# Performance work log

Hardware: AMD Instinct MI355X
Metric: run time of the kernel (lower is better)

Reference implementation:

```python
import math
import jax, jax.numpy as jnp
import numpy as np
from jax import lax

RAY_START, RAY_END = 0.5, 2.5
N_PLANES = 32

# ---- camera constants (faithful to pose_spherical / fibonacci_sphere / ImagePlanes init) ----

def _pose_spherical_np(theta, phi, radius):
    trans_t = np.array([[1,0,0,0],[0,1,0,0],[0,0,1,radius],[0,0,0,1]], dtype=np.float64)
    p = phi/180.0*np.pi
    rot_phi = np.array([[1,0,0,0],[0,np.cos(p),-np.sin(p),0],[0,np.sin(p),np.cos(p),0],[0,0,0,1]], dtype=np.float64)
    t = theta/180.0*np.pi
    rot_theta = np.array([[np.cos(t),0,-np.sin(t),0],[0,1,0,0],[np.sin(t),0,np.cos(t),0],[0,0,0,1]], dtype=np.float64)
    e = 90.0/180.0*np.pi
    rot_eta = np.array([[np.cos(e),np.sin(e),0,0],[-np.sin(e),np.cos(e),0,0],[0,0,1,0],[0,0,0,1]], dtype=np.float64)
    c2w = rot_eta @ (rot_theta @ (rot_phi @ trans_t))
    return np.array([[-1,0,0,0],[0,0,1,0],[0,1,0,0],[0,0,0,1]], dtype=np.float64) @ c2w

def _fibonacci_sphere(n):
    pts = []
    golden = math.pi*(math.sqrt(5.0)-1.0)
    for i in range(n):
        y = 1 - (i/float(n-1))*2
        r = math.sqrt(1-y*y)
        th = golden*i
        x, z = math.cos(th)*r, math.sin(th)*r
        pts.append((math.atan2(z, math.sqrt(x*x+y*y)), math.atan2(y, x)))
    return pts

_poses = np.stack([_pose_spherical_np(theta, phi, -1.307) for phi, theta in _fibonacci_sphere(N_PLANES)])
_flip = np.diag(np.array([-1.0,1.0,1.0,1.0]))
POSES34 = jnp.asarray(np.stack([np.linalg.inv(p @ _flip)[:3] for p in _poses]).astype(np.float32))  # [32,3,4]
KMAT = jnp.asarray(np.array([[1.0254,0,0.5],[0,1.0254,0.5],[0,0,1]], dtype=np.float32))  # [3,3]

# ---- grid_sample(bilinear, zeros, align_corners=False) ----

def _grid_sample(img, grid):
    # img [C,H,W], grid [P,2] (x,y) in [-1,1] -> [C,P]
    C, H, W = img.shape
    ix = ((grid[:, 0] + 1.0)*W - 1.0)*0.5
    iy = ((grid[:, 1] + 1.0)*H - 1.0)*0.5
    x0 = jnp.floor(ix); y0 = jnp.floor(iy)
    wx1 = ix - x0; wy1 = iy - y0
    def tap(xx, yy, w):
        valid = (xx >= 0) & (xx <= W - 1) & (yy >= 0) & (yy <= H - 1)
        xi = jnp.clip(xx, 0, W - 1).astype(jnp.int32)
        yi = jnp.clip(yy, 0, H - 1).astype(jnp.int32)
        return img[:, yi, xi] * (w*valid)[None, :]
    return (tap(x0, y0, (1-wx1)*(1-wy1)) + tap(x0+1, y0, wx1*(1-wy1))
            + tap(x0, y0+1, (1-wx1)*wy1) + tap(x0+1, y0+1, wx1*wy1))

# ---- ImagePlanes.forward ----

def _image_plane_feats(images, points):
    # images [32,3,H,W], points [P,3] -> [P, 96+64]
    P = points.shape[0]
    ph = jnp.concatenate([points, jnp.ones((P, 1), points.dtype)], axis=1)  # [P,4]
    cam = jnp.einsum('kij,pj->kip', POSES34, ph)            # [32,3,P]
    ps = jnp.einsum('ij,kjp->kip', KMAT, cam)                # [32,3,P]
    pix = jnp.clip(ps[:, :2, :] / ps[:, 2:3, :], 0.0, 1.0)*2.0 - 1.0  # [32,2,P]
    grid = jnp.transpose(pix, (0, 2, 1))                     # [32,P,2]
    feats = jax.vmap(_grid_sample)(images, grid)             # [32,3,P]
    feats = jnp.transpose(feats, (2, 0, 1)).reshape(P, -1)   # [P,96] plane-major
    pixflat = jnp.transpose(grid, (1, 0, 2)).reshape(P, -1)  # [P,64]
    return jnp.concatenate([feats, pixflat], axis=1)

# ---- RenderNetwork.forward (only self.net path is used) ----

def _decode(x, W1, b1, W2, b2):
    h = jax.nn.softplus(x @ W1 + b1)
    o = h @ W2 + b2
    rgb = jax.nn.sigmoid(o[..., 1:])*(1.0 + 2*0.001) - 0.001
    return rgb, o[..., 0:1]

# ---- MipRayMarcher2 ----

def _ray_march(colors, densities, depths):
    deltas = depths[:, :, 1:] - depths[:, :, :-1]
    cm = (colors[:, :, :-1] + colors[:, :, 1:])*0.5
    dm = (densities[:, :, :-1] + densities[:, :, 1:])*0.5
    zm = (depths[:, :, :-1] + depths[:, :, 1:])*0.5
    dm = jax.nn.softplus(dm - 1.0)
    alpha = 1.0 - jnp.exp(-dm*deltas)
    shifted = jnp.concatenate([jnp.ones_like(alpha[:, :, :1]), 1.0 - alpha + 1e-10], axis=2)
    weights = alpha * jnp.cumprod(shifted, axis=2)[:, :, :-1]
    rgb = jnp.sum(weights*cm, axis=2)*2.0 - 1.0
    wtot = jnp.sum(weights, axis=2)
    depth = jnp.sum(weights*zm, axis=2)/wtot
    depth = jnp.clip(jnp.where(jnp.isnan(depth), jnp.inf, depth), jnp.min(depths), jnp.max(depths))
    return rgb, depth, weights

# ---- importance sampling (sample_pdf + maxpool/avgpool smoothing) ----

def _sample_pdf(bins, weights, u, eps=1e-5):
    M = weights.shape[-1]
    weights = weights + eps
    pdf = weights / jnp.sum(weights, -1, keepdims=True)
    cdf = jnp.cumsum(pdf, -1)
    cdf = jnp.concatenate([jnp.zeros_like(cdf[:, :1]), cdf], -1)  # [R,M+1]
    inds = jax.vmap(lambda c, uu: jnp.searchsorted(c, uu, side='right'))(cdf, u)
    below = jnp.maximum(inds - 1, 0)
    above = jnp.minimum(inds, M)
    cdf_b = jnp.take_along_axis(cdf, below, 1)
    cdf_a = jnp.take_along_axis(cdf, above, 1)
    bins_b = jnp.take_along_axis(bins, below, 1)
    bins_a = jnp.take_along_axis(bins, above, 1)
    denom = jnp.where(cdf_a - cdf_b < eps, 1.0, cdf_a - cdf_b)
    return bins_b + (u - cdf_b)/denom*(bins_a - bins_b)

def _sample_importance(z_vals, weights, n_imp, u):
    B, N, S, _ = z_vals.shape
    z = z_vals.reshape(B*N, S)
    w = weights.reshape(B*N, S - 1)
    wp = jnp.pad(w, ((0, 0), (1, 1)), constant_values=-jnp.inf)
    m = jnp.maximum(wp[:, :-1], wp[:, 1:])          # max_pool1d(k=2,s=1,p=1)
    sm = (m[:, :-1] + m[:, 1:])*0.5 + 0.01           # avg_pool1d(k=2,s=1)
    samples = _sample_pdf(z, sm[:, 1:-1], u.reshape(B*N, n_imp))
    return lax.stop_gradient(samples).reshape(B, N, n_imp, 1)

# ---- full ImportanceRenderer.forward ----

def _forward(planes, ray_origins, ray_directions, strat_noise, pdf_u, W1, b1, W2, b2, D, n_imp):
    B, N = ray_origins.shape[0], ray_origins.shape[1]
    H, Wd = planes.shape[-2], planes.shape[-1]
    images = planes.reshape(B, N_PLANES, 3, H, Wd)
    delta = (RAY_END - RAY_START)/(D - 1)
    depths_c = jnp.linspace(RAY_START, RAY_END, D, dtype=planes.dtype).reshape(1, 1, D, 1) + strat_noise*delta

    def run_pass(depths):
        S = depths.shape[2]
        pts = (ray_origins[:, :, None, :] + depths*ray_directions[:, :, None, :]).reshape(B, N*S, 3)
        feats = jax.vmap(_image_plane_feats)(images, pts)  # [B,N*S,160]
        rgb, sigma = _decode(feats, W1, b1, W2, b2)
        return rgb.reshape(B, N, S, 32), sigma.reshape(B, N, S, 1)

    colors_c, dens_c = run_pass(depths_c)
    _, _, w_c = _ray_march(colors_c, dens_c, depths_c)
    depths_f = _sample_importance(depths_c, w_c, n_imp, pdf_u)
    colors_f, dens_f = run_pass(depths_f)

    all_d = jnp.concatenate([depths_c, depths_f], axis=2)
    all_c = jnp.concatenate([colors_c, colors_f], axis=2)
    all_s = jnp.concatenate([dens_c, dens_f], axis=2)
    order = jnp.argsort(all_d[..., 0], axis=2)[..., None]
    all_d = jnp.take_along_axis(all_d, order, axis=2)
    all_c = jnp.take_along_axis(all_c, order, axis=2)
    all_s = jnp.take_along_axis(all_s, order, axis=2)
    rgb_final, depth_final, w = _ray_march(all_c, all_s, all_d)
    return jnp.concatenate([rgb_final, depth_final, jnp.sum(w, axis=2)], axis=-1)  # [B,N,34]


def setup_inputs() -> dict:
    key = jax.random.key(0)
    ks = jax.random.split(key, 7)
    B, N, D, NI, H = 2, 4096, 48, 48, 64
    rd = jax.random.normal(ks[2], (B, N, 3), jnp.float32)
    rd = rd / jnp.linalg.norm(rd, axis=-1, keepdims=True)
    return {
        'planes': jax.random.normal(ks[0], (B, 96, H, H), jnp.float32),
        'ray_origins': jax.random.normal(ks[1], (B, N, 3), jnp.float32)*0.1,
        'ray_directions': rd,
        'strat_noise': jax.random.uniform(ks[3], (B, N, D, 1), jnp.float32),
        'pdf_u': jax.random.uniform(ks[4], (B, N, NI), jnp.float32),
        'W1': jax.random.normal(ks[5], (160, 64), jnp.float32)*0.05,
        'b1': jnp.zeros((64,), jnp.float32),
        'W2': jax.random.normal(ks[6], (64, 33), jnp.float32)*0.05,
        'b2': jnp.zeros((33,), jnp.float32),
        'depth_resolution': 48,
        'N_importance': 48,
    }


def reference(planes, ray_origins, ray_directions, strat_noise, pdf_u, W1, b1, W2, b2, depth_resolution, N_importance):
    return _forward(planes, ray_origins, ray_directions, strat_noise, pdf_u, W1, b1, W2, b2, depth_resolution, N_importance)
```

## Files before the change

### kernel.cpp

```cpp
#include <hip/hip_runtime.h>
#include <math.h>

#define B_   2
#define N_   4096
#define S_   48
#define NPL  32
#define NRAYS (B_*N_)
#define NPTS  (NRAYS*S_)
#define DELTA_ (2.0f/47.0f)
#define NBLK_FUSED (NPTS/256)

#define QT_XS    66
#define QT_YS    65
#define QT_PLANE (QT_YS*QT_XS)
#define QT_TOTAL (64*QT_PLANE)
#define SETUP_GRID (2 + 64 + NPTS/256)

#define OFF_POSES  0
#define OFF_MINMAX 384
#define OFF_W1E    512
#define OFF_W2E    8704
#define OFF_B2E    10240
#define OFF_ST     16384
#define OFF_PTS    2212864
#define OFF_DC     3785728
#define OFF_DF     4178944
#define OFF_SC     4572160
#define OFF_SF     4965376
#define OFF_CC     5358592
#define OFF_CF     11650048

typedef __attribute__((ext_vector_type(8))) short short8;
typedef __attribute__((ext_vector_type(4))) float f32x4;

__device__ __forceinline__ float softplus_f(float x) {
    return fmaxf(x, 0.f) + __logf(1.f + __expf(-fabsf(x)));
}
__device__ __forceinline__ float sigmoid_f(float x) {
    return __builtin_amdgcn_rcpf(1.f + __expf(-x));
}
__device__ __forceinline__ unsigned short bf16rne(float x) {
    unsigned u = __float_as_uint(x);
    u += 0x7FFFu + ((u >> 16) & 1u);
    return (unsigned short)(u >> 16);
}
__device__ __forceinline__ unsigned bf16pk(float lo, float hi) {
    return (unsigned)bf16rne(lo) | ((unsigned)bf16rne(hi) << 16);
}
__device__ __forceinline__ float bf2f(unsigned short v) {
    return __uint_as_float(((unsigned)v) << 16);
}
__device__ __forceinline__ float bflo(unsigned u) { return __uint_as_float(u << 16); }
__device__ __forceinline__ float bfhi(unsigned u) { return __uint_as_float(u & 0xffff0000u); }

__device__ void mul3(const double* a, const double* b, double* o) {
    for (int i = 0; i < 3; i++)
        for (int j = 0; j < 3; j++) {
            double s = 0.0;
            for (int k = 0; k < 3; k++) s += a[i*3+k]*b[k*3+j];
            o[i*3+j] = s;
        }
}

__global__ __launch_bounds__(256) void k_setup(
    float* ws, const float* __restrict__ W1,
    const float* __restrict__ W2, const float* __restrict__ b2,
    const float* __restrict__ planes, const float* __restrict__ noise,
    const float* __restrict__ ro, const float* __restrict__ rd)
{
    __shared__ unsigned short texs[3][4096];
    __shared__ float smn[4], smx[4];
    int bid = blockIdx.x;
    int t = threadIdx.x;
    if (bid == 0) {
        if (t < 32) {
            double y = 1.0 - (t/31.0)*2.0;
            double rr = sqrt(fmax(1.0 - y*y, 0.0));
            double golden = M_PI*(sqrt(5.0) - 1.0);
            double th = golden*(double)t;
            double x = cos(th)*rr, z = sin(th)*rr;
            double phi   = atan2(z, sqrt(x*x + y*y));
            double theta = atan2(y, x);
            double p  = phi/180.0*M_PI;
            double tt = theta/180.0*M_PI;
            double e  = 90.0/180.0*M_PI;
            double cp = cos(p), sp = sin(p), ct = cos(tt), st = sin(tt);
            double ce = cos(e), se = sin(e);
            double Ph[9] = {1,0,0,  0,cp,-sp,  0,sp,cp};
            double Th[9] = {ct,0,-st,  0,1,0,  st,0,ct};
            double Et[9] = {ce,se,0,  -se,ce,0,  0,0,1};
            double M3[9] = {-1,0,0,  0,0,1,  0,1,0};
            double A[9], Bm[9], R[9];
            mul3(Th, Ph, A);
            mul3(Et, A, Bm);
            mul3(M3, Bm, R);
            double radius = -1.307;
            double tv0 = radius*R[2], tv1 = radius*R[5], tv2 = radius*R[8];
            double Rf[9] = {-R[0],R[1],R[2], -R[3],R[4],R[5], -R[6],R[7],R[8]};
            float* P = ws + OFF_POSES + t*12;
            for (int j = 0; j < 3; j++) {
                double r0 = Rf[0*3+j], r1 = Rf[1*3+j], r2 = Rf[2*3+j];
                P[j*4+0] = (float)r0;
                P[j*4+1] = (float)r1;
                P[j*4+2] = (float)r2;
                P[j*4+3] = (float)(-(r0*tv0 + r1*tv1 + r2*tv2));
            }
        }
        unsigned short* w1e = (unsigned short*)(ws + OFF_W1E);
        for (int idx = t; idx < 64*256; idx += 256) {
            int n = idx >> 8, k = idx & 255;
            int p = k >> 3, f = k & 7;
            float v = 0.f;
            if (f < 3)      v = W1[(3*p+f)*64 + n];
            else if (f < 5) v = W1[(96 + 2*p + (f-3))*64 + n];
            w1e[idx] = bf16rne(v);
        }
        unsigned short* w2e = (unsigned short*)(ws + OFF_W2E);
        for (int idx = t; idx < 48*64; idx += 256) {
            int n = idx >> 6, k = idx & 63;
            float v = (n < 33) ? W2[k*33 + n] : 0.f;
            w2e[idx] = bf16rne(v);
        }
        for (int idx = t; idx < 48; idx += 256)
            ws[OFF_B2E + idx] = (idx < 33) ? b2[idx] : 0.f;
    } else if (bid == 1) {
        float mn = 1e30f, mx = -1e30f;
        for (int r = t; r < NRAYS; r += 256) {
            float n0  = noise[(size_t)r*48];
            float n47 = noise[(size_t)r*48 + 47];
            mn = fminf(mn, 0.5f + n0*DELTA_);
            mx = fmaxf(mx, 0.5f + 47.f*DELTA_ + n47*DELTA_);
        }
        for (int off = 32; off > 0; off >>= 1) {
            mn = fminf(mn, __shfl_down(mn, off));
            mx = fmaxf(mx, __shfl_down(mx, off));
        }
        if ((t & 63) == 0) { smn[t >> 6] = mn; smx[t >> 6] = mx; }
        __syncthreads();
        if (t == 0) {
            ws[OFF_MINMAX]     = fminf(fminf(smn[0], smn[1]), fminf(smn[2], smn[3]));
            ws[OFF_MINMAX + 1] = fmaxf(fmaxf(smx[0], smx[1]), fmaxf(smx[2], smx[3]));
        }
    } else if (bid < 66) {
        int bp = bid - 2;
        int b = bp >> 5, p = bp & 31;
        const float* base = planes + ((size_t)b*96 + 3*p)*4096;
        for (int i = t; i < 4096; i += 256) {
            texs[0][i] = bf16rne(base[i]);
            texs[1][i] = bf16rne(base[4096 + i]);
            texs[2][i] = bf16rne(base[8192 + i]);
        }
        __syncthreads();
        uint4* qd = (uint4*)(ws + OFF_ST) + (size_t)bp*QT_PLANE*2;
        for (int e = t; e < QT_PLANE; e += 256) {
            int y0 = e / QT_XS, x0 = e - y0*QT_XS;
            unsigned short cs[4][3] = {{0,0,0},{0,0,0},{0,0,0},{0,0,0}};
            if (x0 <= 64) {
#pragma unroll
                for (int dy = 0; dy < 2; dy++) {
                    int jy = y0 - 1 + dy;
                    if (jy < 0 || jy > 63) continue;
#pragma unroll
                    for (int dx = 0; dx < 2; dx++) {
                        int jx = x0 - 1 + dx;
                        if (jx < 0 || jx > 63) continue;
                        int ti = jy*64 + jx;
                        cs[dy*2+dx][0] = texs[0][ti];
                        cs[dy*2+dx][1] = texs[1][ti];
                        cs[dy*2+dx][2] = texs[2][ti];
                    }
                }
            }
            uint4 qa, qb;
            qa.x = (unsigned)cs[0][0] | ((unsigned)cs[0][1] << 16);
            qa.y = (unsigned)cs[0][2] | ((unsigned)cs[1][0] << 16);
            qa.z = (unsigned)cs[1][1] | ((unsigned)cs[1][2] << 16);
            qa.w = (unsigned)cs[2][0] | ((unsigned)cs[2][1] << 16);
            qb.x = (unsigned)cs[2][2] | ((unsigned)cs[3][0] << 16);
            qb.y = (unsigned)cs[3][1] | ((unsigned)cs[3][2] << 16);
            qb.z = 0u; qb.w = 0u;
            qd[(size_t)e*2]     = qa;
            qd[(size_t)e*2 + 1] = qb;
        }
    } else {
        int pt = (bid - 66)*256 + t;
        int ray = pt / S_;
        int j = pt - ray*S_;
        float depth = 0.5f + (float)j*DELTA_ + noise[pt]*DELTA_;
        ws[OFF_DC + pt] = depth;
        float px = fmaf(depth, rd[ray*3+0], ro[ray*3+0]);
        float py = fmaf(depth, rd[ray*3+1], ro[ray*3+1]);
        float pz = fmaf(depth, rd[ray*3+2], ro[ray*3+2]);
        ((float4*)(ws + OFF_PTS))[pt] = make_float4(px, py, pz, depth);
    }
}

__device__ __forceinline__ void proj_load(
    const f32x4 Pa, const f32x4 Pb, const f32x4 Pc,
    const uint4* __restrict__ stp, float px, float py, float pz,
    uint4& qa, uint2& qb, float& wx, float& wy, unsigned& gpk)
{
    float c0 = fmaf(Pa.x,px, fmaf(Pa.y,py, fmaf(Pa.z,pz, Pa.w)));
    float c1 = fmaf(Pb.x,px, fmaf(Pb.y,py, fmaf(Pb.z,pz, Pb.w)));
    float c2 = fmaf(Pc.x,px, fmaf(Pc.y,py, fmaf(Pc.z,pz, Pc.w)));
    float rz = __builtin_amdgcn_rcpf(c2);
    float gx = fminf(fmaxf((1.0254f*c0 + 0.5f*c2)*rz, 0.f), 1.f)*2.f - 1.f;
    float gy = fminf(fmaxf((1.0254f*c1 + 0.5f*c2)*rz, 0.f), 1.f)*2.f - 1.f;
    float ixp = ((gx + 1.f)*64.f - 1.f)*0.5f + 1.f;
    float iyp = ((gy + 1.f)*64.f - 1.f)*0.5f + 1.f;
    float xf = floorf(ixp), yf = floorf(iyp);
    wx = ixp - xf; wy = iyp - yf;
    int x0p = (int)xf, y0p = (int)yf;
    const uint4* ep = stp + (unsigned)(y0p*QT_XS + x0p)*2u;
    qa = ep[0];
    qb = *(const uint2*)(ep + 1);
    gpk = bf16pk(gx, gy);
}

__device__ __forceinline__ void bilerp_pack(
    const uint4 qa, const uint2 qb, float wx, float wy, unsigned gpk, uint4& av)
{
    float wy0 = 1.f - wy, wy1 = wy;
    float w0x = 1.f - wx, w1x = wx;
    float tl0 = fmaf(wy0, bflo(qa.x), wy1*bflo(qa.w));
    float tl1 = fmaf(wy0, bfhi(qa.x), wy1*bfhi(qa.w));
    float tl2 = fmaf(wy0, bflo(qa.y), wy1*bflo(qb.x));
    float tr0 = fmaf(wy0, bfhi(qa.y), wy1*bfhi(qb.x));
    float tr1 = fmaf(wy0, bflo(qa.z), wy1*bflo(qb.y));
    float tr2 = fmaf(wy0, bfhi(qa.z), wy1*bfhi(qb.y));
    float f0 = fmaf(w0x, tl0, w1x*tr0);
    float f1 = fmaf(w0x, tl1, w1x*tr1);
    float f2 = fmaf(w0x, tl2, w1x*tr2);
    av.x = bf16pk(f0, f1);
    av.y = ((unsigned)bf16rne(f2)) | (gpk << 16);
    av.z = gpk >> 16;
    av.w = 0u;
}

__global__ __launch_bounds__(256) void k_fused(
    const uint4* __restrict__ stq, const float4* __restrict__ pts,
    const float* __restrict__ poses,
    const float* __restrict__ b1, const unsigned short* __restrict__ w1e,
    const unsigned short* __restrict__ w2e, const float* __restrict__ b2e,
    unsigned short* __restrict__ colors, float* __restrict__ dens)
{
    __shared__ __align__(16) unsigned short smem[4][1152];
    __shared__ __align__(16) float pl[384];
    int tid = threadIdx.x;
    int wv = tid >> 6, lane = tid & 63;
    int n = lane & 15, q = lane >> 4;
    int bid = blockIdx.x;
    int swz = (bid & 7)*(NBLK_FUSED/8) + (bid >> 3);
    int wlocal = swz*256 + wv*64;
    int bq = (wlocal >= NPTS/2) ? 32 : 0;

    for (int i = tid; i < 384; i += 256) pl[i] = poses[i];
    __syncthreads();

    float px[4], py[4], pz[4];
#pragma unroll
    for (int t = 0; t < 4; t++) {
        float4 pv = pts[wlocal + t*16 + n];
        px[t] = pv.x; py[t] = pv.y; pz[t] = pv.z;
    }

    f32x4 acc[4][4];
#pragma unroll
    for (int t = 0; t < 4; t++)
#pragma unroll
        for (int nt = 0; nt < 4; nt++) {
            float bv = b1[nt*16 + n];
            acc[t][nt] = (f32x4){bv, bv, bv, bv};
        }

#pragma unroll
    for (int s = 0; s < 8; s++) {
        int plane = s*4 + q;
        const f32x4* Pq = (const f32x4*)(pl + plane*12);
        f32x4 Pa = Pq[0], Pb = Pq[1], Pc = Pq[2];
        const uint4* stp = stq + (unsigned)(bq + plane)*(unsigned)(QT_PLANE*2);
        union { short8 s8; uint4 u; } av[4];
        {
            uint4 qa0, qa1; uint2 qb0, qb1;
            float wxa, wya, wxb, wyb; unsigned g0, g1;
            proj_load(Pa, Pb, Pc, stp, px[0], py[0], pz[0], qa0, qb0, wxa, wya, g0);
            proj_load(Pa, Pb, Pc, stp, px[1], py[1], pz[1], qa1, qb1, wxb, wyb, g1);
            bilerp_pack(qa0, qb0, wxa, wya, g0, av[0].u);
            bilerp_pack(qa1, qb1, wxb, wyb, g1, av[1].u);
            proj_load(Pa, Pb, Pc, stp, px[2], py[2], pz[2], qa0, qb0, wxa, wya, g0);
            proj_load(Pa, Pb, Pc, stp, px[3], py[3], pz[3], qa1, qb1, wxb, wyb, g1);
            bilerp_pack(qa0, qb0, wxa, wya, g0, av[2].u);
            bilerp_pack(qa1, qb1, wxb, wyb, g1, av[3].u);
        }
#pragma unroll
        for (int nt = 0; nt < 4; nt++) {
            short8 bfw = *(const short8*)(w1e + (nt*16 + n)*256 + s*32 + q*8);
#pragma unroll
            for (int t = 0; t < 4; t++)
                acc[t][nt] = __builtin_amdgcn_mfma_f32_16x16x32_bf16(av[t].s8, bfw, acc[t][nt], 0, 0, 0);
        }
    }

    short8 b2f[3][2];
#pragma unroll
    for (int nt = 0; nt < 3; nt++)
#pragma unroll
        for (int s2 = 0; s2 < 2; s2++)
            b2f[nt][s2] = *(const short8*)(w2e + (nt*16 + n)*64 + s2*32 + q*8);

    unsigned short* ht = &smem[wv][0];
#pragma unroll
    for (int t = 0; t < 4; t++) {
#pragma unroll
        for (int nt = 0; nt < 4; nt++)
#pragma unroll
            for (int r = 0; r < 4; r++) {
                float hv = softplus_f(acc[t][nt][r]);
                ht[(q*4 + r)*72 + nt*16 + n] = bf16rne(hv);
            }
        short8 a2[2];
#pragma unroll
        for (int s2 = 0; s2 < 2; s2++)
            a2[s2] = *(const short8*)(ht + n*72 + s2*32 + q*8);

        f32x4 acc2[3];
#pragma unroll
        for (int nt = 0; nt < 3; nt++) {
            float bv = b2e[nt*16 + n];
            acc2[nt] = (f32x4){bv, bv, bv, bv};
        }
#pragma unroll
        for (int nt = 0; nt < 3; nt++)
#pragma unroll
            for (int s2 = 0; s2 < 2; s2++)
                acc2[nt] = __builtin_amdgcn_mfma_f32_16x16x32_bf16(a2[s2], b2f[nt][s2], acc2[nt], 0, 0, 0);

        float* ot = (float*)ht;
#pragma unroll
        for (int nt = 0; nt < 3; nt++) {
            int col = nt*16 + n;
#pragma unroll
            for (int r = 0; r < 4; r++) {
                float v = acc2[nt][r];
                int row = q*4 + r;
                if (col == 0) ot[row*34 + 32] = v;
                else if (col <= 32) {
                    float sg = sigmoid_f(v);
                    ot[row*34 + (col-1)] = fmaf(sg, 1.002f, -0.001f);
                }
            }
        }
        unsigned* cgu = (unsigned*)(colors + (size_t)(wlocal + t*16)*32);
#pragma unroll
        for (int i = 0; i < 4; i++) {
            int ui = i*64 + lane;
            int pt = ui >> 4, ch = (ui & 15)*2;
            cgu[ui] = bf16pk(ot[pt*34 + ch], ot[pt*34 + ch + 1]);
        }
        if (lane < 16) dens[wlocal + t*16 + lane] = ot[lane*34 + 32];
    }
}

__global__ __launch_bounds__(256) void k_imp(const float* __restrict__ u, float* ws,
                                             const float* __restrict__ ro,
                                             const float* __restrict__ rd,
                                             float4* __restrict__ pts) {
    __shared__ float zl[4][48];
    __shared__ float cdfl[4][46];
    int tid = threadIdx.x;
    int wv = tid >> 6, lane = tid & 63;
    int r = blockIdx.x*4 + wv;
    const float* z   = ws + OFF_DC + (size_t)r*48;
    const float* den = ws + OFF_SC + (size_t)r*48;
    float zv = 0.f, dv = 0.f;
    if (lane < 48) { zv = z[lane]; dv = den[lane]; zl[wv][lane] = zv; }
    float zn  = __shfl_down(zv, 1);
    float dnn = __shfl_down(dv, 1);
    float alpha = 0.f, f = 1.f;
    if (lane < 47) {
        float sp = softplus_f(0.5f*(dv + dnn) - 1.f);
        alpha = 1.f - __expf(-sp*(zn - zv));
        f = 1.f - alpha + 1e-10f;
    }
    float v = f;
    for (int off = 1; off < 64; off <<= 1) { float o = __shfl_up(v, off); if (lane >= off) v *= o; }
    float T = __shfl_up(v, 1); if (lane == 0) T = 1.f;
    float w = alpha*T;
    float wn1 = __shfl_down(w, 1), wn2 = __shfl_down(w, 2);
    float pw = 0.f;
    if (lane < 45) pw = 0.5f*(fmaxf(w, wn1) + fmaxf(wn1, wn2)) + 0.01f + 1e-5f;
    float s = pw;
    for (int off = 1; off < 64; off <<= 1) { float o = __shfl_up(s, off); if (lane >= off) s += o; }
    float csum = __shfl(s, 63);
    if (lane < 45) cdfl[wv][lane+1] = s/csum;
    if (lane == 63) cdfl[wv][0] = 0.f;
    __syncthreads();
    if (lane < 48) {
        float uu = u[(size_t)r*48 + lane];
        int lo = 0, hi = 46;
        while (lo < hi) { int mid = (lo+hi)>>1; if (uu >= cdfl[wv][mid]) lo = mid+1; else hi = mid; }
        int below = max(lo-1, 0), above = min(lo, 45);
        float cb = cdfl[wv][below], ca = cdfl[wv][above];
        float zb = zl[wv][below],   za = zl[wv][above];
        float dn2 = ca - cb; if (dn2 < 1e-5f) dn2 = 1.f;
        float df_s = zb + (uu - cb)/dn2*(za - zb);
        ws[OFF_DF + (size_t)r*48 + lane] = df_s;
        float fx = fmaf(df_s, rd[r*3+0], ro[r*3+0]);
        float fy = fmaf(df_s, rd[r*3+1], ro[r*3+1]);
        float fz = fmaf(df_s, rd[r*3+2], ro[r*3+2]);
        pts[(size_t)r*48 + lane] = make_float4(fx, fy, fz, df_s);
    }
}

__global__ __launch_bounds__(256) void k_final(float* __restrict__ out, const float* __restrict__ ws,
                                               const unsigned short* __restrict__ cC,
                                               const unsigned short* __restrict__ cF)
{
    __shared__ float kd[4][96];
    __shared__ float kden[4][96];
    __shared__ float sdl[4][96];
    __shared__ float sdenl[4][96];
    __shared__ int   sidxl[4][96];
    __shared__ float warr[4][96];
    __shared__ float earr[4][96];
    int tid = threadIdx.x;
    int wv = tid >> 6, lane = tid & 63;
    int r = blockIdx.x*4 + wv;
    const float* dc = ws + OFF_DC + (size_t)r*48;
    const float* df = ws + OFF_DF + (size_t)r*48;
    const float* sc = ws + OFF_SC + (size_t)r*48;
    const float* sf = ws + OFF_SF + (size_t)r*48;
    for (int i = lane; i < 96; i += 64) {
        float d, dn;
        if (i < 48) { d = dc[i]; dn = sc[i]; }
        else        { d = df[i-48]; dn = sf[i-48]; }
        kd[wv][i] = d; kden[wv][i] = dn;
    }
    __syncthreads();
    for (int i = lane; i < 96; i += 64) {
        float d = kd[wv][i];
        int rank = 0;
        for (int j = 0; j < 96; j++) {
            float dj = kd[wv][j];
            rank += (int)((dj < d) | ((dj == d) & (j < i)));
        }
        sdl[wv][rank] = d; sdenl[wv][rank] = kden[wv][i]; sidxl[wv][rank] = i;
    }
    __syncthreads();
    int i2 = 2*lane;
    float a0=0.f, f0=1.f, a1=0.f, f1=1.f, d0=0.f, d1=0.f, d2=0.f;
    if (i2 < 95) {
        d0 = sdl[wv][i2]; d1 = sdl[wv][i2+1];
        float sp = softplus_f(0.5f*(sdenl[wv][i2] + sdenl[wv][i2+1]) - 1.f);
        a0 = 1.f - __expf(-sp*(d1 - d0)); f0 = 1.f - a0 + 1e-10f;
    }
    if (i2+1 < 95) {
        d2 = sdl[wv][i2+2];
        float sp = softplus_f(0.5f*(sdenl[wv][i2+1] + sdenl[wv][i2+2]) - 1.f);
        a1 = 1.f - __expf(-sp*(d2 - d1)); f1 = 1.f - a1 + 1e-10f;
    }
    float p = f0*f1, v = p;
    for (int off = 1; off < 64; off <<= 1) { float o = __shfl_up(v, off); if (lane >= off) v *= o; }
    float excl = __shfl_up(v, 1); if (lane == 0) excl = 1.f;
    float w0 = a0*excl, w1 = a1*excl*f0;
    if (i2   < 96) warr[wv][i2]   = w0;
    if (i2+1 < 96) warr[wv][i2+1] = w1;
    float wsm = w0 + w1;
    float dsm = w0*0.5f*(d0+d1) + w1*0.5f*(d1+d2);
    for (int off = 32; off; off >>= 1) { wsm += __shfl_xor(wsm, off); dsm += __shfl_xor(dsm, off); }
    __syncthreads();
    for (int i = lane; i < 96; i += 64) {
        float wp = (i > 0)  ? warr[wv][i-1] : 0.f;
        float wc = (i < 95) ? warr[wv][i]   : 0.f;
        earr[wv][sidxl[wv][i]] = 0.5f*(wp + wc);
    }
    __syncthreads();
    int ch = lane & 31, half = lane >> 5;
    const unsigned short* cbase = (half ? cF : cC) + ((size_t)r*48)*32 + ch;
    const float* eb = &earr[wv][half*48];
    float a = 0.f;
    for (int jj = 0; jj < 48; jj++)
        a = fmaf(eb[jj], bf2f(cbase[(size_t)jj*32]), a);
    a += __shfl_xor(a, 32);
    if (lane < 32) out[(size_t)r*34 + lane] = 2.f*a - 1.f;
    if (lane == 0) {
        float gmn = ws[OFF_MINMAX];
        float gmx = ws[OFF_MINMAX + 1];
        float depth = dsm/wsm;
        if (depth != depth) depth = __builtin_inff();
        depth = fminf(fmaxf(depth, gmn), gmx);
        out[(size_t)r*34 + 32] = depth;
        out[(size_t)r*34 + 33] = wsm;
    }
}

extern "C" void kernel_launch(void* const* d_in, const int* in_sizes, int n_in,
                              void* d_out, int out_size, void* d_ws, size_t ws_size,
                              hipStream_t stream) {
    const float* planes = (const float*)d_in[0];
    const float* ro     = (const float*)d_in[1];
    const float* rd     = (const float*)d_in[2];
    const float* noise  = (const float*)d_in[3];
    const float* u      = (const float*)d_in[4];
    const float* W1     = (const float*)d_in[5];
    const float* b1     = (const float*)d_in[6];
    const float* W2     = (const float*)d_in[7];
    const float* b2     = (const float*)d_in[8];
    float* ws  = (float*)d_ws;
    float* out = (float*)d_out;
    const unsigned short* w1e = (const unsigned short*)(ws + OFF_W1E);
    const unsigned short* w2e = (const unsigned short*)(ws + OFF_W2E);
    const uint4* stq = (const uint4*)(ws + OFF_ST);
    float4* pts = (float4*)(ws + OFF_PTS);
    unsigned short* cC = (unsigned short*)(ws + OFF_CC);
    unsigned short* cF = (unsigned short*)(ws + OFF_CF);

    hipLaunchKernelGGL(k_setup, dim3(SETUP_GRID), dim3(256), 0, stream,
                       ws, W1, W2, b2, planes, noise, ro, rd);
    hipLaunchKernelGGL(k_fused, dim3(NBLK_FUSED), dim3(256), 0, stream,
                       stq, pts, ws + OFF_POSES, b1, w1e, w2e, ws + OFF_B2E, cC, ws + OFF_SC);
    hipLaunchKernelGGL(k_imp, dim3(NRAYS/4), dim3(256), 0, stream, u, ws, ro, rd, pts);
    hipLaunchKernelGGL(k_fused, dim3(NBLK_FUSED), dim3(256), 0, stream,
                       stq, pts, ws + OFF_POSES, b1, w1e, w2e, ws + OFF_B2E, cF, ws + OFF_SF);
    hipLaunchKernelGGL(k_final, dim3(NRAYS/4), dim3(256), 0, stream, out, ws, cC, cF);
}
```

Measured before the change: 268.7 us.

## Store plane texels as compact padded grid and halve points per block

```diff
diff --git a/kernel.cpp b/kernel.cpp
--- a/kernel.cpp
+++ b/kernel.cpp
@@ -8,12 +8,11 @@
 #define NRAYS (B_*N_)
 #define NPTS  (NRAYS*S_)
 #define DELTA_ (2.0f/47.0f)
-#define NBLK_FUSED (NPTS/256)
-
-#define QT_XS    66
-#define QT_YS    65
-#define QT_PLANE (QT_YS*QT_XS)
-#define QT_TOTAL (64*QT_PLANE)
+#define NBLK_FUSED (NPTS/128)
+
+#define ST_XS    66
+#define ST_YS    66
+#define ST_PLANE (ST_YS*ST_XS)
 #define SETUP_GRID (2 + 64 + NPTS/256)
 
 #define OFF_POSES  0
@@ -22,13 +21,13 @@
 #define OFF_W2E    8704
 #define OFF_B2E    10240
 #define OFF_ST     16384
-#define OFF_PTS    2212864
-#define OFF_DC     3785728
-#define OFF_DF     4178944
-#define OFF_SC     4572160
-#define OFF_SF     4965376
-#define OFF_CC     5358592
-#define OFF_CF     11650048
+#define OFF_PTS    573952
+#define OFF_DC     2146816
+#define OFF_DF     2540032
+#define OFF_SC     2933248
+#define OFF_SF     3326464
+#define OFF_CC     3719680
+#define OFF_CF     10011136
 
 typedef __attribute__((ext_vector_type(8))) short short8;
 typedef __attribute__((ext_vector_type(4))) float f32x4;
@@ -151,36 +150,16 @@
             texs[2][i] = bf16rne(base[8192 + i]);
         }
         __syncthreads();
-        uint4* qd = (uint4*)(ws + OFF_ST) + (size_t)bp*QT_PLANE*2;
-        for (int e = t; e < QT_PLANE; e += 256) {
-            int y0 = e / QT_XS, x0 = e - y0*QT_XS;
-            unsigned short cs[4][3] = {{0,0,0},{0,0,0},{0,0,0},{0,0,0}};
-            if (x0 <= 64) {
-#pragma unroll
-                for (int dy = 0; dy < 2; dy++) {
-                    int jy = y0 - 1 + dy;
-                    if (jy < 0 || jy > 63) continue;
-#pragma unroll
-                    for (int dx = 0; dx < 2; dx++) {
-                        int jx = x0 - 1 + dx;
-                        if (jx < 0 || jx > 63) continue;
-                        int ti = jy*64 + jx;
-                        cs[dy*2+dx][0] = texs[0][ti];
-                        cs[dy*2+dx][1] = texs[1][ti];
-                        cs[dy*2+dx][2] = texs[2][ti];
-                    }
-                }
+        uint2* qd = (uint2*)(ws + OFF_ST) + (size_t)bp*ST_PLANE;
+        for (int e = t; e < ST_PLANE; e += 256) {
+            int j = e / ST_XS, i = e - j*ST_XS;
+            unsigned ux = 0, uy = 0;
+            if (j >= 1 && j <= 64 && i >= 1 && i <= 64) {
+                int ti = (j-1)*64 + (i-1);
+                ux = (unsigned)texs[0][ti] | ((unsigned)texs[1][ti] << 16);
+                uy = (unsigned)texs[2][ti];
             }
-            uint4 qa, qb;
-            qa.x = (unsigned)cs[0][0] | ((unsigned)cs[0][1] << 16);
-            qa.y = (unsigned)cs[0][2] | ((unsigned)cs[1][0] << 16);
-            qa.z = (unsigned)cs[1][1] | ((unsigned)cs[1][2] << 16);
-            qa.w = (unsigned)cs[2][0] | ((unsigned)cs[2][1] << 16);
-            qb.x = (unsigned)cs[2][2] | ((unsigned)cs[3][0] << 16);
-            qb.y = (unsigned)cs[3][1] | ((unsigned)cs[3][2] << 16);
-            qb.z = 0u; qb.w = 0u;
-            qd[(size_t)e*2]     = qa;
-            qd[(size_t)e*2 + 1] = qb;
+            qd[e] = make_uint2(ux, uy);
         }
     } else {
         int pt = (bid - 66)*256 + t;
@@ -195,39 +174,39 @@
     }
 }
 
-__device__ __forceinline__ void proj_load(
+__device__ __forceinline__ void proj_pt(
     const f32x4 Pa, const f32x4 Pb, const f32x4 Pc,
-    const uint4* __restrict__ stp, float px, float py, float pz,
-    uint4& qa, uint2& qb, float& wx, float& wy, unsigned& gpk)
+    float px, float py, float pz,
+    int& eoff, float& wx, float& wy, unsigned& gpk)
 {
     float c0 = fmaf(Pa.x,px, fmaf(Pa.y,py, fmaf(Pa.z,pz, Pa.w)));
     float c1 = fmaf(Pb.x,px, fmaf(Pb.y,py, fmaf(Pb.z,pz, Pb.w)));
     float c2 = fmaf(Pc.x,px, fmaf(Pc.y,py, fmaf(Pc.z,pz, Pc.w)));
     float rz = __builtin_amdgcn_rcpf(c2);
-    float gx = fminf(fmaxf((1.0254f*c0 + 0.5f*c2)*rz, 0.f), 1.f)*2.f - 1.f;
-    float gy = fminf(fmaxf((1.0254f*c1 + 0.5f*c2)*rz, 0.f), 1.f)*2.f - 1.f;
-    float ixp = ((gx + 1.f)*64.f - 1.f)*0.5f + 1.f;
-    float iyp = ((gy + 1.f)*64.f - 1.f)*0.5f + 1.f;
+    float cx = fminf(fmaxf((1.0254f*c0 + 0.5f*c2)*rz, 0.f), 1.f);
+    float cy = fminf(fmaxf((1.0254f*c1 + 0.5f*c2)*rz, 0.f), 1.f);
+    float gx = fmaf(2.f, cx, -1.f);
+    float gy = fmaf(2.f, cy, -1.f);
+    float ixp = fmaf(64.f, cx, 0.5f);
+    float iyp = fmaf(64.f, cy, 0.5f);
     float xf = floorf(ixp), yf = floorf(iyp);
     wx = ixp - xf; wy = iyp - yf;
-    int x0p = (int)xf, y0p = (int)yf;
-    const uint4* ep = stp + (unsigned)(y0p*QT_XS + x0p)*2u;
-    qa = ep[0];
-    qb = *(const uint2*)(ep + 1);
+    eoff = (int)yf*ST_XS + (int)xf;
     gpk = bf16pk(gx, gy);
 }
 
 __device__ __forceinline__ void bilerp_pack(
-    const uint4 qa, const uint2 qb, float wx, float wy, unsigned gpk, uint4& av)
+    const uint2 e00, const uint2 e01, const uint2 e10, const uint2 e11,
+    float wx, float wy, unsigned gpk, uint4& av)
 {
     float wy0 = 1.f - wy, wy1 = wy;
     float w0x = 1.f - wx, w1x = wx;
-    float tl0 = fmaf(wy0, bflo(qa.x), wy1*bflo(qa.w));
-    float tl1 = fmaf(wy0, bfhi(qa.x), wy1*bfhi(qa.w));
-    float tl2 = fmaf(wy0, bflo(qa.y), wy1*bflo(qb.x));
-    float tr0 = fmaf(wy0, bfhi(qa.y), wy1*bfhi(qb.x));
-    float tr1 = fmaf(wy0, bflo(qa.z), wy1*bflo(qb.y));
-    float tr2 = fmaf(wy0, bfhi(qa.z), wy1*bfhi(qb.y));
+    float tl0 = fmaf(wy0, bflo(e00.x), wy1*bflo(e10.x));
+    float tl1 = fmaf(wy0, bfhi(e00.x), wy1*bfhi(e10.x));
+    float tl2 = fmaf(wy0, bflo(e00.y), wy1*bflo(e10.y));
+    float tr0 = fmaf(wy0, bflo(e01.x), wy1*bflo(e11.x));
+    float tr1 = fmaf(wy0, bfhi(e01.x), wy1*bfhi(e11.x));
+    float tr2 = fmaf(wy0, bflo(e01.y), wy1*bflo(e11.y));
     float f0 = fmaf(w0x, tl0, w1x*tr0);
     float f1 = fmaf(w0x, tl1, w1x*tr1);
     float f2 = fmaf(w0x, tl2, w1x*tr2);
@@ -237,8 +216,8 @@
     av.w = 0u;
 }
 
-__global__ __launch_bounds__(256) void k_fused(
-    const uint4* __restrict__ stq, const float4* __restrict__ pts,
+__global__ __launch_bounds__(256, 4) void k_fused(
+    const uint2* __restrict__ stq, const float4* __restrict__ pts,
     const float* __restrict__ poses,
     const float* __restrict__ b1, const unsigned short* __restrict__ w1e,
     const unsigned short* __restrict__ w2e, const float* __restrict__ b2e,
@@ -251,22 +230,22 @@
     int n = lane & 15, q = lane >> 4;
     int bid = blockIdx.x;
     int swz = (bid & 7)*(NBLK_FUSED/8) + (bid >> 3);
-    int wlocal = swz*256 + wv*64;
+    int wlocal = swz*128 + wv*32;
     int bq = (wlocal >= NPTS/2) ? 32 : 0;
 
     for (int i = tid; i < 384; i += 256) pl[i] = poses[i];
     __syncthreads();
 
-    float px[4], py[4], pz[4];
-#pragma unroll
-    for (int t = 0; t < 4; t++) {
+    float px[2], py[2], pz[2];
+#pragma unroll
+    for (int t = 0; t < 2; t++) {
         float4 pv = pts[wlocal + t*16 + n];
         px[t] = pv.x; py[t] = pv.y; pz[t] = pv.z;
     }
 
-    f32x4 acc[4][4];
-#pragma unroll
-    for (int t = 0; t < 4; t++)
+    f32x4 acc[2][4];
+#pragma unroll
+    for (int t = 0; t < 2; t++)
 #pragma unroll
         for (int nt = 0; nt < 4; nt++) {
             float bv = b1[nt*16 + n];
@@ -278,25 +257,24 @@
         int plane = s*4 + q;
         const f32x4* Pq = (const f32x4*)(pl + plane*12);
         f32x4 Pa = Pq[0], Pb = Pq[1], Pc = Pq[2];
-        const uint4* stp = stq + (unsigned)(bq + plane)*(unsigned)(QT_PLANE*2);
-        union { short8 s8; uint4 u; } av[4];
+        const uint2* stp = stq + (unsigned)(bq + plane)*(unsigned)ST_PLANE;
+        union { short8 s8; uint4 u; } av[2];
         {
-            uint4 qa0, qa1; uint2 qb0, qb1;
-            float wxa, wya, wxb, wyb; unsigned g0, g1;
-            proj_load(Pa, Pb, Pc, stp, px[0], py[0], pz[0], qa0, qb0, wxa, wya, g0);
-            proj_load(Pa, Pb, Pc, stp, px[1], py[1], pz[1], qa1, qb1, wxb, wyb, g1);
-            bilerp_pack(qa0, qb0, wxa, wya, g0, av[0].u);
-            bilerp_pack(qa1, qb1, wxb, wyb, g1, av[1].u);
-            proj_load(Pa, Pb, Pc, stp, px[2], py[2], pz[2], qa0, qb0, wxa, wya, g0);
-            proj_load(Pa, Pb, Pc, stp, px[3], py[3], pz[3], qa1, qb1, wxb, wyb, g1);
-            bilerp_pack(qa0, qb0, wxa, wya, g0, av[2].u);
-            bilerp_pack(qa1, qb1, wxb, wyb, g1, av[3].u);
+            int eo0, eo1; float wx0, wy0, wx1, wy1; unsigned g0, g1;
+            proj_pt(Pa, Pb, Pc, px[0], py[0], pz[0], eo0, wx0, wy0, g0);
+            proj_pt(Pa, Pb, Pc, px[1], py[1], pz[1], eo1, wx1, wy1, g1);
+            const uint2* e0 = stp + eo0;
+            const uint2* e1 = stp + eo1;
+            uint2 a00 = e0[0], a01 = e0[1], a10 = e0[ST_XS], a11 = e0[ST_XS+1];
+            uint2 b00 = e1[0], b01 = e1[1], b10 = e1[ST_XS], b11 = e1[ST_XS+1];
+            bilerp_pack(a00, a01, a10, a11, wx0, wy0, g0, av[0].u);
+            bilerp_pack(b00, b01, b10, b11, wx1, wy1, g1, av[1].u);
         }
 #pragma unroll
         for (int nt = 0; nt < 4; nt++) {
             short8 bfw = *(const short8*)(w1e + (nt*16 + n)*256 + s*32 + q*8);
 #pragma unroll
-            for (int t = 0; t < 4; t++)
+            for (int t = 0; t < 2; t++)
                 acc[t][nt] = __builtin_amdgcn_mfma_f32_16x16x32_bf16(av[t].s8, bfw, acc[t][nt], 0, 0, 0);
         }
     }
@@ -310,7 +288,7 @@
 
     unsigned short* ht = &smem[wv][0];
 #pragma unroll
-    for (int t = 0; t < 4; t++) {
+    for (int t = 0; t < 2; t++) {
 #pragma unroll
         for (int nt = 0; nt < 4; nt++)
 #pragma unroll
@@ -510,7 +488,7 @@
     float* out = (float*)d_out;
     const unsigned short* w1e = (const unsigned short*)(ws + OFF_W1E);
     const unsigned short* w2e = (const unsigned short*)(ws + OFF_W2E);
-    const uint4* stq = (const uint4*)(ws + OFF_ST);
+    const uint2* stq = (const uint2*)(ws + OFF_ST);
     float4* pts = (float4*)(ws + OFF_PTS);
     unsigned short* cC = (unsigned short*)(ws + OFF_CC);
     unsigned short* cF = (unsigned short*)(ws + OFF_CF);
```

Result: slower. 275.3 us (+2.5%).
